# Optimization experiments

Measured on AMD Instinct MI355X. Metric: run time of the kernel, lower is better.

The kernel has to match this reference:

```python
import jax, jax.numpy as jnp
import numpy as np
import math

H = 256
NH = 8
HD = H // NH
FF = 2 * H
NSESS = 8
LN_EPS = 1e-5


def _layernorm(x, g, b):
    m = jnp.mean(x, axis=-1, keepdims=True)
    v = jnp.mean((x - m) ** 2, axis=-1, keepdims=True)
    return (x - m) / jnp.sqrt(v + LN_EPS) * g + b


def setup_inputs() -> dict:
    key = jax.random.key(0)
    ks = jax.random.split(key, 32)
    B, S, N = 4, 256, 32
    inp = {
        'sequence': jax.random.normal(ks[0], (B, S, N, H), dtype=jnp.float32),
        'regime_signal': jax.random.normal(ks[1], (B, S), dtype=jnp.float32),
        'session_transition': jax.random.normal(ks[2], (B, S), dtype=jnp.float32),
    }
    w = lambda k, shape: jax.random.normal(k, shape, dtype=jnp.float32) * 0.02
    inp['q_w'] = w(ks[3], (H, H)); inp['q_b'] = jnp.zeros((H,), jnp.float32)
    inp['k_w'] = w(ks[4], (H, H)); inp['k_b'] = jnp.zeros((H,), jnp.float32)
    inp['v_w'] = w(ks[5], (H, H)); inp['v_b'] = jnp.zeros((H,), jnp.float32)
    inp['o_w'] = w(ks[6], (H, H)); inp['o_b'] = jnp.zeros((H,), jnp.float32)
    inp['sess_emb'] = w(ks[7], (NSESS, H))
    inp['reg_w'] = w(ks[8], (H,)); inp['reg_b'] = jnp.zeros((H,), jnp.float32)
    inp['tr_w'] = w(ks[9], (H,)); inp['tr_b'] = jnp.zeros((H,), jnp.float32)
    inp['tq_w'] = w(ks[10], (H, H)); inp['tq_b'] = jnp.zeros((H,), jnp.float32)
    inp['tk_w'] = w(ks[11], (H, H)); inp['tk_b'] = jnp.zeros((H,), jnp.float32)
    inp['ff_w1'] = w(ks[12], (H, FF)); inp['ff_b1'] = jnp.zeros((FF,), jnp.float32)
    inp['ff_w2'] = w(ks[13], (FF, H)); inp['ff_b2'] = jnp.zeros((H,), jnp.float32)
    inp['ln1_g'] = jnp.ones((H,), jnp.float32); inp['ln1_b'] = jnp.zeros((H,), jnp.float32)
    inp['ln2_g'] = jnp.ones((H,), jnp.float32); inp['ln2_b'] = jnp.zeros((H,), jnp.float32)
    inp['valid_mask'] = jax.random.randint(ks[14], (B, S, N), 0, 2).astype(bool)
    inp['session_codes'] = jax.random.randint(ks[15], (B, S), 0, NSESS).astype(jnp.int64)
    return inp


def _forward(sequence, regime_signal, session_transition,
             q_w, q_b, k_w, k_b, v_w, v_b, o_w, o_b,
             sess_emb, reg_w, reg_b, tr_w, tr_b,
             tq_w, tq_b, tk_w, tk_b,
             ff_w1, ff_b1, ff_w2, ff_b2,
             ln1_g, ln1_b, ln2_g, ln2_b,
             valid_mask, session_codes):
    B, S, N, Hd = sequence.shape
    BN = B * N
    # [B,S,N,H] -> [B*N, S, H]
    flat = sequence.transpose(0, 2, 1, 3).reshape(BN, S, Hd)

    # time-state: session embedding + regime/transition scalar projections
    sess = jnp.clip(session_codes, 0, NSESS - 1)
    sess_flat = jnp.broadcast_to(sess[:, None, :], (B, N, S)).reshape(BN, S)
    time_state = sess_emb[sess_flat]  # [BN, S, H]
    reg_flat = jnp.broadcast_to(regime_signal[:, None, :], (B, N, S)).reshape(BN, S)
    time_state = time_state + reg_flat[..., None] * reg_w + reg_b
    tr_flat = jnp.broadcast_to(session_transition[:, None, :], (B, N, S)).reshape(BN, S)
    time_state = time_state + tr_flat[..., None] * tr_w + tr_b

    def heads(x):  # [BN,S,H] -> [BN,NH,S,HD]
        return x.reshape(BN, S, NH, HD).transpose(0, 2, 1, 3)

    q = heads((flat + time_state) @ q_w + q_b)
    k = heads((flat + time_state) @ k_w + k_b)
    v = heads(flat @ v_w + v_b)
    tq = heads(time_state @ tq_w + tq_b)
    tk = heads(time_state @ tk_w + tk_b)

    scale = 1.0 / math.sqrt(float(HD))
    scores = jnp.einsum('bhqd,bhkd->bhqk', q, k) * scale
    scores = scores + 0.25 * jnp.einsum('bhqd,bhkd->bhqk', tq, tk) * scale

    causal = jnp.triu(jnp.ones((S, S), dtype=bool), k=1)
    scores = jnp.where(causal[None, None], -10000.0, scores)

    valid = valid_mask.transpose(0, 2, 1).reshape(BN, S)  # [BN,S]
    all_invalid = ~jnp.any(valid, axis=1)  # [BN]
    scores = jnp.where(~valid[:, None, None, :], -10000.0, scores)
    first_key = (jnp.arange(S) == 0)
    scores = jnp.where(all_invalid[:, None, None, None] & first_key, 0.0, scores)

    attn = jax.nn.softmax(scores, axis=-1)
    attn = attn * valid[:, None, None, :].astype(attn.dtype)
    attn = attn / jnp.maximum(jnp.sum(attn, axis=-1, keepdims=True), 1e-6)
    attn = jnp.where(all_invalid[:, None, None, None], 0.0, attn)

    attn_out = jnp.einsum('bhqk,bhkd->bhqd', attn, v)
    attn_out = attn_out.transpose(0, 2, 1, 3).reshape(BN, S, Hd)
    attn_out = attn_out @ o_w + o_b

    x = _layernorm(flat + attn_out, ln1_g, ln1_b)  # dropout identity (eval / p=0)
    ff = jax.nn.gelu(x @ ff_w1 + ff_b1, approximate=False) @ ff_w2 + ff_b2
    x = _layernorm(x + ff, ln2_g, ln2_b)
    x = x * valid[..., None].astype(x.dtype)
    return x.reshape(B, N, S, Hd).transpose(0, 2, 1, 3)  # [B,S,N,H]


def reference(sequence, regime_signal, session_transition,
              q_w, q_b, k_w, k_b, v_w, v_b, o_w, o_b,
              sess_emb, reg_w, reg_b, tr_w, tr_b,
              tq_w, tq_b, tk_w, tk_b,
              ff_w1, ff_b1, ff_w2, ff_b2,
              ln1_g, ln1_b, ln2_g, ln2_b,
              valid_mask, session_codes):
    return _forward(sequence, regime_signal, session_transition,
                    q_w, q_b, k_w, k_b, v_w, v_b, o_w, o_b,
                    sess_emb, reg_w, reg_b, tr_w, tr_b,
                    tq_w, tq_b, tk_w, tk_b,
                    ff_w1, ff_b1, ff_w2, ff_b2,
                    ln1_g, ln1_b, ln2_g, ln2_b,
                    valid_mask, session_codes)
```

## Files before the change

### kernel.cpp

```cpp
#include <hip/hip_runtime.h>
#include <math.h>

#define B_ 4
#define S_ 256
#define N_ 32
#define H_ 256
#define NH_ 8
#define HD_ 32
#define FF_ 512
#define BN_ 128
#define M_ 32768
#define BS_ 1024

typedef __attribute__((ext_vector_type(8))) short short8;
typedef __attribute__((ext_vector_type(4))) short short4v;
typedef __attribute__((ext_vector_type(4))) float f32x4;
typedef __attribute__((ext_vector_type(16))) float f32x16;
typedef __attribute__((ext_vector_type(4))) int i32x4;

__device__ __forceinline__ unsigned short f2bf(float f) {
  unsigned u = __builtin_bit_cast(unsigned, f);
  u = (u + 0x7FFFu + ((u >> 16) & 1u)) >> 16;
  return (unsigned short)u;
}
__device__ __forceinline__ float bf2f(unsigned short h) {
  unsigned u = ((unsigned)h) << 16;
  return __builtin_bit_cast(float, u);
}

__device__ __forceinline__ void gload16(const void* g, void* l) {
  __builtin_amdgcn_global_load_lds(
      (const __attribute__((address_space(1))) unsigned*)g,
      (__attribute__((address_space(3))) unsigned*)l, 16, 0, 0);
}

__global__ __launch_bounds__(256)
void cvtts_kernel(const float* __restrict__ q_w, const float* __restrict__ k_w,
                  const float* __restrict__ v_w, const float* __restrict__ o_w,
                  const float* __restrict__ tq_w, const float* __restrict__ tk_w,
                  const float* __restrict__ ff1_w, const float* __restrict__ ff2_w,
                  unsigned short* __restrict__ wqk, unsigned short* __restrict__ wv,
                  unsigned short* __restrict__ wo, unsigned short* __restrict__ wtqtk,
                  unsigned short* __restrict__ wff1, unsigned short* __restrict__ wff2,
                  const float* __restrict__ reg, const float* __restrict__ tr,
                  const int* __restrict__ codes, const float* __restrict__ semb,
                  const float* __restrict__ reg_w, const float* __restrict__ reg_b,
                  const float* __restrict__ tr_w, const float* __restrict__ tr_b,
                  float* __restrict__ ts) {
  const int bid = blockIdx.x, tid = threadIdx.x;
  if (bid >= 2560) {
    const int bs = bid - 2560;
    int c = codes[bs];
    c = c < 0 ? 0 : (c > 7 ? 7 : c);
    const float r = reg[bs], t = tr[bs];
    ts[bs * H_ + tid] = semb[c * H_ + tid] + r * reg_w[tid] + reg_b[tid]
                        + t * tr_w[tid] + tr_b[tid];
    return;
  }
  const float* src; unsigned short* dst; int ns, K, base;
  if (bid < 256)       { src = q_w;   dst = wqk;           ns = 8; K = 256; base = 0; }
  else if (bid < 512)  { src = k_w;   dst = wqk + 65536;   ns = 8; K = 256; base = 256; }
  else if (bid < 768)  { src = v_w;   dst = wv;            ns = 8; K = 256; base = 512; }
  else if (bid < 1024) { src = o_w;   dst = wo;            ns = 8; K = 256; base = 768; }
  else if (bid < 1280) { src = tq_w;  dst = wtqtk;         ns = 8; K = 256; base = 1024; }
  else if (bid < 1536) { src = tk_w;  dst = wtqtk + 65536; ns = 8; K = 256; base = 1280; }
  else if (bid < 2048) { src = ff1_w; dst = wff1;          ns = 9; K = 256; base = 1536; }
  else                 { src = ff2_w; dst = wff2;          ns = 8; K = 512; base = 2048; }
  const int idx = (bid - base) * 256 + tid;
  const int k = idx >> ns, n = idx & ((1 << ns) - 1);
  dst[n * K + k] = f2bf(src[idx]);
}

__global__ __launch_bounds__(256)
void prep_kernel(const float* __restrict__ seq, const float* __restrict__ ts,
                 unsigned short* __restrict__ flatb, unsigned short* __restrict__ fpb) {
  const int row = blockIdx.x * 8 + (threadIdx.x >> 5);
  const int c0 = (threadIdx.x & 31) * 8;
  const int bn = row >> 8, s = row & 255;
  const int b = bn >> 5, n = bn & 31;
  const float* sp = &seq[((((b << 8) + s) << 5) + n) * 256 + c0];
  const float* tp = &ts[(((b << 8) + s) << 8) + c0];
  const float4 a0 = *(const float4*)sp, a1 = *(const float4*)(sp + 4);
  const float4 t0 = *(const float4*)tp, t1 = *(const float4*)(tp + 4);
  short8 fv, gv;
  fv[0] = (short)f2bf(a0.x); fv[1] = (short)f2bf(a0.y);
  fv[2] = (short)f2bf(a0.z); fv[3] = (short)f2bf(a0.w);
  fv[4] = (short)f2bf(a1.x); fv[5] = (short)f2bf(a1.y);
  fv[6] = (short)f2bf(a1.z); fv[7] = (short)f2bf(a1.w);
  gv[0] = (short)f2bf(a0.x + t0.x); gv[1] = (short)f2bf(a0.y + t0.y);
  gv[2] = (short)f2bf(a0.z + t0.z); gv[3] = (short)f2bf(a0.w + t0.w);
  gv[4] = (short)f2bf(a1.x + t1.x); gv[5] = (short)f2bf(a1.y + t1.y);
  gv[6] = (short)f2bf(a1.z + t1.z); gv[7] = (short)f2bf(a1.w + t1.w);
  *(short8*)&flatb[row * 256 + c0] = fv;
  *(short8*)&fpb[row * 256 + c0] = gv;
}

__global__ __launch_bounds__(256)
void proj_kernel(const unsigned short* __restrict__ fpb,
                 const unsigned short* __restrict__ flatb,
                 const float* __restrict__ ts,
                 const unsigned short* __restrict__ wqk,
                 const unsigned short* __restrict__ wv,
                 const unsigned short* __restrict__ wtqtk,
                 const float* __restrict__ q_b, const float* __restrict__ k_b,
                 const float* __restrict__ v_b,
                 const float* __restrict__ tq_b, const float* __restrict__ tk_b,
                 unsigned short* __restrict__ qkb, unsigned short* __restrict__ vb,
                 unsigned short* __restrict__ tqtkb, float c2) {
  __shared__ unsigned short As[128 * 64];
  __shared__ unsigned short Bs[128 * 64];
  const int bid = blockIdx.x, tid = threadIdx.x;
  const int l = tid & 63, w = tid >> 6;
  const int wr = w >> 1, wc = w & 1;
  const int lr = l & 15, lg = l >> 4;

  int region, m0, n0, NOUT;
  const unsigned short* Ab = nullptr;
  const float* Af = nullptr;
  const unsigned short* Wt;
  const float* b0; const float* b1;
  unsigned short* Cv; float scl;
  if (bid < 1024) {
    region = 0; m0 = (bid & 255) * 128; n0 = (bid >> 8) * 128; NOUT = 512;
    Ab = fpb; Wt = wqk; b0 = q_b; b1 = k_b; Cv = qkb; scl = c2;
  } else if (bid < 1536) {
    const int idx = bid - 1024;
    region = 1; m0 = (idx & 255) * 128; n0 = (idx >> 8) * 128; NOUT = 256;
    Ab = flatb; Wt = wv; b0 = v_b; b1 = v_b; Cv = vb; scl = 1.0f;
  } else {
    const int idx = bid - 1536;
    region = 2; m0 = (idx & 7) * 128; n0 = (idx >> 3) * 128; NOUT = 512;
    Af = ts; Wt = wtqtk; b0 = tq_b; b1 = tk_b; Cv = tqtkb; scl = 0.25f * c2;
  }

  f32x4 acc[4][4] = {};
  const unsigned short* ga = (region != 2)
      ? Ab + (m0 + w * 32 + (l >> 3)) * 256 + (l & 7) * 8 : nullptr;
  const unsigned short* gb = Wt + (n0 + w * 32 + (l >> 3)) * 256 + (l & 7) * 8;

  for (int k0 = 0; k0 < 256; k0 += 64) {
    if (region != 2) {
#pragma unroll
      for (int i = 0; i < 4; ++i)
        gload16(ga + k0 + i * 8 * 256, &As[(w * 32 + i * 8) * 64]);
    } else {
#pragma unroll
      for (int i = 0; i < 8; ++i) {
        const int seg = i * 256 + tid;
        const int r = seg >> 4, c4 = (seg & 15) * 4;
        const float4 a4 = *(const float4*)&Af[(m0 + r) * 256 + k0 + c4];
        short4v sv;
        sv[0] = (short)f2bf(a4.x); sv[1] = (short)f2bf(a4.y);
        sv[2] = (short)f2bf(a4.z); sv[3] = (short)f2bf(a4.w);
        *(short4v*)&As[r * 64 + c4] = sv;
      }
    }
#pragma unroll
    for (int i = 0; i < 4; ++i)
      gload16(gb + k0 + i * 8 * 256, &Bs[(w * 32 + i * 8) * 64]);
    __syncthreads();
#pragma unroll
    for (int ks = 0; ks < 2; ++ks) {
      short8 af[4], bfr[4];
#pragma unroll
      for (int qt = 0; qt < 4; ++qt)
        af[qt] = *(const short8*)&As[(wr * 64 + qt * 16 + lr) * 64 + ks * 32 + lg * 8];
#pragma unroll
      for (int nt = 0; nt < 4; ++nt)
        bfr[nt] = *(const short8*)&Bs[(wc * 64 + nt * 16 + lr) * 64 + ks * 32 + lg * 8];
#pragma unroll
      for (int qt = 0; qt < 4; ++qt)
#pragma unroll
        for (int nt = 0; nt < 4; ++nt)
          acc[qt][nt] = __builtin_amdgcn_mfma_f32_16x16x32_bf16(
              af[qt], bfr[nt], acc[qt][nt], 0, 0, 0);
    }
    __syncthreads();
  }

#pragma unroll
  for (int qt = 0; qt < 4; ++qt) {
#pragma unroll
    for (int nt = 0; nt < 4; ++nt) {
      const int col = n0 + wc * 64 + nt * 16 + lr;
      const float bsv = (col < 256) ? b0[col] : b1[col - 256];
      const float sc = (col < 256) ? scl : 1.0f;
#pragma unroll
      for (int i = 0; i < 4; ++i) {
        const int row = m0 + wr * 64 + qt * 16 + (lg << 2) + i;
        Cv[row * NOUT + col] = f2bf((acc[qt][nt][i] + bsv) * sc);
      }
    }
  }
}

template<int K, int NOUT>
__global__ __launch_bounds__(256)
void mmb_kernel(const unsigned short* __restrict__ Ab,
                const unsigned short* __restrict__ Wt,
                const float* __restrict__ bias,
                unsigned short* __restrict__ Cv) {
  __shared__ unsigned short As[128 * 64];
  __shared__ unsigned short Bs[128 * 64];
  const int tid = threadIdx.x;
  const int m0 = blockIdx.x * 128, n0 = blockIdx.y * 128;
  const int l = tid & 63, w = tid >> 6;
  const int wr = w >> 1, wc = w & 1;
  const int lr = l & 15, lg = l >> 4;
  f32x4 acc[4][4] = {};

  const unsigned short* ga = Ab + (m0 + w * 32 + (l >> 3)) * K + (l & 7) * 8;
  const unsigned short* gb = Wt + (n0 + w * 32 + (l >> 3)) * K + (l & 7) * 8;

  for (int k0 = 0; k0 < K; k0 += 64) {
#pragma unroll
    for (int i = 0; i < 4; ++i) {
      gload16(ga + k0 + i * 8 * K, &As[(w * 32 + i * 8) * 64]);
      gload16(gb + k0 + i * 8 * K, &Bs[(w * 32 + i * 8) * 64]);
    }
    __syncthreads();
#pragma unroll
    for (int ks = 0; ks < 2; ++ks) {
      short8 af[4], bfr[4];
#pragma unroll
      for (int qt = 0; qt < 4; ++qt)
        af[qt] = *(const short8*)&As[(wr * 64 + qt * 16 + lr) * 64 + ks * 32 + lg * 8];
#pragma unroll
      for (int nt = 0; nt < 4; ++nt)
        bfr[nt] = *(const short8*)&Bs[(wc * 64 + nt * 16 + lr) * 64 + ks * 32 + lg * 8];
#pragma unroll
      for (int qt = 0; qt < 4; ++qt)
#pragma unroll
        for (int nt = 0; nt < 4; ++nt)
          acc[qt][nt] = __builtin_amdgcn_mfma_f32_16x16x32_bf16(
              af[qt], bfr[nt], acc[qt][nt], 0, 0, 0);
    }
    __syncthreads();
  }

#pragma unroll
  for (int qt = 0; qt < 4; ++qt) {
#pragma unroll
    for (int nt = 0; nt < 4; ++nt) {
      const int col = n0 + wc * 64 + nt * 16 + lr;
      const float bsv = bias[col];
#pragma unroll
      for (int i = 0; i < 4; ++i) {
        const int row = m0 + wr * 64 + qt * 16 + (lg << 2) + i;
        float v = acc[qt][nt][i] + bsv;
        v = 0.5f * v * (1.0f + erff(v * 0.70710678118654752f));
        Cv[row * NOUT + col] = f2bf(v);
      }
    }
  }
}

template<int K, bool FINAL>
__global__ __launch_bounds__(256, 2)
void gemmln_kernel(const unsigned short* __restrict__ Ab,
                   const unsigned short* __restrict__ Wt,
                   const float* __restrict__ bias,
                   const unsigned short* __restrict__ resb,
                   const float* __restrict__ g, const float* __restrict__ bb,
                   const int* __restrict__ valid,
                   void* __restrict__ out) {
  __shared__ unsigned short As[64 * 64];
  __shared__ unsigned short Bs[256 * 64];
  __shared__ float Red[4][64][2];
  const int tid = threadIdx.x;
  const int m0 = blockIdx.x * 64;
  const int l = tid & 63, w = tid >> 6;
  const int lr = l & 15, lg = l >> 4;
  f32x4 acc[4][4] = {};

  const unsigned short* ga = Ab + (m0 + w * 16 + (l >> 3)) * K + (l & 7) * 8;
  const unsigned short* gb = Wt + (w * 64 + (l >> 3)) * K + (l & 7) * 8;

  for (int k0 = 0; k0 < K; k0 += 64) {
#pragma unroll
    for (int i = 0; i < 2; ++i)
      gload16(ga + k0 + i * 8 * K, &As[(w * 16 + i * 8) * 64]);
#pragma unroll
    for (int i = 0; i < 8; ++i)
      gload16(gb + k0 + i * 8 * K, &Bs[(w * 64 + i * 8) * 64]);
    __syncthreads();
#pragma unroll
    for (int ks = 0; ks < 2; ++ks) {
      short8 af[4], bfr[4];
#pragma unroll
      for (int qt = 0; qt < 4; ++qt)
        af[qt] = *(const short8*)&As[(qt * 16 + lr) * 64 + ks * 32 + lg * 8];
#pragma unroll
      for (int nt = 0; nt < 4; ++nt)
        bfr[nt] = *(const short8*)&Bs[(w * 64 + nt * 16 + lr) * 64 + ks * 32 + lg * 8];
#pragma unroll
      for (int qt = 0; qt < 4; ++qt)
#pragma unroll
        for (int nt = 0; nt < 4; ++nt)
          acc[qt][nt] = __builtin_amdgcn_mfma_f32_16x16x32_bf16(
              af[qt], bfr[nt], acc[qt][nt], 0, 0, 0);
    }
    __syncthreads();
  }

#pragma unroll
  for (int qt = 0; qt < 4; ++qt) {
#pragma unroll
    for (int i = 0; i < 4; ++i) {
      const int rl = qt * 16 + (lg << 2) + i;
      const int row = m0 + rl;
      float s1 = 0.0f, s2 = 0.0f;
#pragma unroll
      for (int nt = 0; nt < 4; ++nt) {
        const int col = w * 64 + nt * 16 + lr;
        float v = acc[qt][nt][i] + bias[col] + bf2f(resb[row * 256 + col]);
        acc[qt][nt][i] = v;
        s1 += v; s2 += v * v;
      }
      s1 += __shfl_xor(s1, 1); s2 += __shfl_xor(s2, 1);
      s1 += __shfl_xor(s1, 2); s2 += __shfl_xor(s2, 2);
      s1 += __shfl_xor(s1, 4); s2 += __shfl_xor(s2, 4);
      s1 += __shfl_xor(s1, 8); s2 += __shfl_xor(s2, 8);
      if (lr == 0) { Red[w][rl][0] = s1; Red[w][rl][1] = s2; }
    }
  }
  __syncthreads();

#pragma unroll
  for (int qt = 0; qt < 4; ++qt) {
#pragma unroll
    for (int i = 0; i < 4; ++i) {
      const int rl = qt * 16 + (lg << 2) + i;
      const int row = m0 + rl;
      const float s1 = (Red[0][rl][0] + Red[1][rl][0])
                     + (Red[2][rl][0] + Red[3][rl][0]);
      const float s2 = (Red[0][rl][1] + Red[1][rl][1])
                     + (Red[2][rl][1] + Red[3][rl][1]);
      const float mean = s1 * (1.0f / 256.0f);
      const float var = s2 * (1.0f / 256.0f) - mean * mean;
      const float rstd = rsqrtf(var + 1e-5f);
      if (FINAL) {
        const int bn = row >> 8, s = row & 255;
        const int b = bn >> 5, n = bn & 31;
        const float vm = (valid[((b << 8) + s) * 32 + n] != 0) ? 1.0f : 0.0f;
        float* op = (float*)out + ((((b << 8) + s) << 5) + n) * 256;
#pragma unroll
        for (int nt = 0; nt < 4; ++nt) {
          const int col = w * 64 + nt * 16 + lr;
          op[col] = ((acc[qt][nt][i] - mean) * rstd * g[col] + bb[col]) * vm;
        }
      } else {
        unsigned short* op = (unsigned short*)out + row * 256;
#pragma unroll
        for (int nt = 0; nt < 4; ++nt) {
          const int col = w * 64 + nt * 16 + lr;
          op[col] = f2bf((acc[qt][nt][i] - mean) * rstd * g[col] + bb[col]);
        }
      }
    }
  }
}

__device__ __forceinline__ void attn_group(
    const int kbase, const int qa, const int hi, const int lq,
    const short8* __restrict__ qf,
    const char* __restrict__ KsB, const char* __restrict__ VsB,
    const unsigned long long bm0, const unsigned long long bm1,
    const unsigned long long bm2, const unsigned long long bm3,
    f32x16& oacc, float& lrun) {
  f32x16 s = {};
#pragma unroll
  for (int df = 0; df < 4; ++df) {
    const int key = kbase + lq;
    const short8 akf = *(const short8*)(
        KsB + key * 128 + ((df * 32 + hi * 16) ^ ((key & 7) << 4)));
    s = __builtin_amdgcn_mfma_f32_32x32x16_bf16(akf, qf[df], s, 0, 0, 0);
  }
  const unsigned long long bmc = (kbase < 64) ? bm0 : (kbase < 128) ? bm1
                               : (kbase < 192) ? bm2 : bm3;
  const unsigned wnd = (kbase & 32) ? (unsigned)(bmc >> 32) : (unsigned)bmc;
  float p[16];
#pragma unroll
  for (int r = 0; r < 16; ++r) {
    const int crow = (r & 3) + 8 * (r >> 2) + 4 * hi;
    const int key = kbase + crow;
    const bool ok = (key <= qa) && (((wnd >> crow) & 1u) != 0u);
    p[r] = ok ? __builtin_amdgcn_exp2f(s[r]) : 0.0f;
  }
  float rs = ((p[0] + p[1]) + (p[2] + p[3])) + ((p[4] + p[5]) + (p[6] + p[7]))
           + ((p[8] + p[9]) + (p[10] + p[11])) + ((p[12] + p[13]) + (p[14] + p[15]));
  rs += __shfl_xor(rs, 32);
  lrun += rs;
  unsigned wds[8];
#pragma unroll
  for (int i2 = 0; i2 < 8; ++i2)
    wds[i2] = (unsigned)f2bf(p[2 * i2]) | ((unsigned)f2bf(p[2 * i2 + 1]) << 16);
  unsigned xw[8];
#pragma unroll
  for (int i2 = 0; i2 < 8; ++i2)
    xw[i2] = (unsigned)__shfl_xor((int)wds[i2], 32);
  i32x4 f0, f1;
  f0[0] = (int)(hi ? xw[2] : wds[0]);
  f0[1] = (int)(hi ? xw[3] : wds[1]);
  f0[2] = (int)(hi ? wds[2] : xw[0]);
  f0[3] = (int)(hi ? wds[3] : xw[1]);
  f1[0] = (int)(hi ? xw[6] : wds[4]);
  f1[1] = (int)(hi ? xw[7] : wds[5]);
  f1[2] = (int)(hi ? wds[6] : xw[4]);
  f1[3] = (int)(hi ? wds[7] : xw[5]);
  const short8 pf0 = __builtin_bit_cast(short8, f0);
  const short8 pf1 = __builtin_bit_cast(short8, f1);
  {
    const short8 avf = *(const short8*)(
        VsB + lq * 512 + (((kbase + hi * 8) * 2) ^ ((lq & 7) << 4)));
    oacc = __builtin_amdgcn_mfma_f32_32x32x16_bf16(avf, pf0, oacc, 0, 0, 0);
  }
  {
    const short8 avf = *(const short8*)(
        VsB + lq * 512 + (((kbase + 16 + hi * 8) * 2) ^ ((lq & 7) << 4)));
    oacc = __builtin_amdgcn_mfma_f32_32x32x16_bf16(avf, pf1, oacc, 0, 0, 0);
  }
}

__global__ __launch_bounds__(512, 4)
void attn6_kernel(const unsigned short* __restrict__ qkb,
                  const unsigned short* __restrict__ vb,
                  const unsigned short* __restrict__ tqtkb,
                  const int* __restrict__ valid,
                  unsigned short* __restrict__ ao) {
  __shared__ __align__(16) char KsB[256 * 128];
  __shared__ __align__(16) char VsB[32 * 512];

  const int bn = blockIdx.x & 127;
  const int h = blockIdx.x >> 7;
  const int b = bn >> 5, n = bn & 31;
  const int tid = threadIdx.x, l = tid & 63, w = tid >> 6;
  const int lq = l & 31, hi = l >> 5;
  const int qa = w * 32 + lq;

  const unsigned long long bm0 = __ballot(valid[((b << 8) + 0   + l) * 32 + n] != 0);
  const unsigned long long bm1 = __ballot(valid[((b << 8) + 64  + l) * 32 + n] != 0);
  const unsigned long long bm2 = __ballot(valid[((b << 8) + 128 + l) * 32 + n] != 0);
  const unsigned long long bm3 = __ballot(valid[((b << 8) + 192 + l) * 32 + n] != 0);

  short8 qf[4];
  {
    const unsigned short* qp = &qkb[((bn << 8) + qa) * 512 + (h << 5)];
    const unsigned short* tp = &tqtkb[((b << 8) + qa) * 512 + (h << 5)];
    qf[0] = *(const short8*)&qp[hi * 8];
    qf[1] = *(const short8*)&qp[16 + hi * 8];
    qf[2] = *(const short8*)&tp[hi * 8];
    qf[3] = *(const short8*)&tp[16 + hi * 8];
  }

  {
    const int cp = (l & 7) ^ (l >> 3);
    const unsigned short* base0 = (cp < 4)
        ? &qkb[((bn << 8) + (l >> 3)) * 512 + 256 + (h << 5) + cp * 8]
        : &tqtkb[((b << 8) + (l >> 3)) * 512 + 256 + (h << 5) + (cp - 4) * 8];
#pragma unroll
    for (int i = 0; i < 4; ++i) {
      const int kb0 = i * 64 + w * 8;
      gload16(base0 + kb0 * 512, KsB + kb0 * 128);
    }
  }
#pragma unroll
  for (int i = 0; i < 2; ++i) {
    const int e = i * 512 + tid;
    const int key = e >> 2, c = e & 3;
    const short8 v = *(const short8*)&vb[((bn << 8) + key) * 256 + (h << 5) + c * 8];
#pragma unroll
    for (int j = 0; j < 8; ++j) {
      const int dv = c * 8 + j;
      *(unsigned short*)(VsB + dv * 512 + ((key * 2) ^ ((dv & 7) << 4))) =
          (unsigned short)v[j];
    }
  }
  __syncthreads();

  f32x16 oacc = {}, oacc2 = {};
  float lrun = 0.0f, lrun2 = 0.0f;

  const int gstart = (w >= 4) ? (w - 3) : 0;
  for (int g = gstart; g <= w; ++g)
    attn_group(g << 5, qa, hi, lq, qf, KsB, VsB, bm0, bm1, bm2, bm3, oacc, lrun);

  if (w < 4) {
    const int ch = 7 - w;
    const int qa2 = ch * 32 + lq;
    short8 qf2[4];
    const unsigned short* qp = &qkb[((bn << 8) + qa2) * 512 + (h << 5)];
    const unsigned short* tp = &tqtkb[((b << 8) + qa2) * 512 + (h << 5)];
    qf2[0] = *(const short8*)&qp[hi * 8];
    qf2[1] = *(const short8*)&qp[16 + hi * 8];
    qf2[2] = *(const short8*)&tp[hi * 8];
    qf2[3] = *(const short8*)&tp[16 + hi * 8];
    for (int g = 0; g <= ch - 4; ++g)
      attn_group(g << 5, qa2, hi, lq, qf2, KsB, VsB, bm0, bm1, bm2, bm3,
                 oacc2, lrun2);
  }

  __syncthreads();
  if (w < 4) {
    float* mo = (float*)(KsB + w * 4096);
#pragma unroll
    for (int r = 0; r < 16; ++r) mo[r * 64 + l] = oacc2[r];
    ((float*)(KsB + 16384))[w * 64 + l] = lrun2;
  }
  __syncthreads();
  if (w >= 4) {
    const float* mo = (const float*)(KsB + (7 - w) * 4096);
#pragma unroll
    for (int r = 0; r < 16; ++r) oacc[r] += mo[r * 64 + l];
    lrun += ((const float*)(KsB + 16384))[(7 - w) * 64 + l];
  }

  const float inv = 1.0f / fmaxf(lrun, 1e-6f);
  const int row = (bn << 8) + qa;
#pragma unroll
  for (int g2 = 0; g2 < 4; ++g2) {
    const unsigned long long h0 = f2bf(oacc[4 * g2 + 0] * inv);
    const unsigned long long h1 = f2bf(oacc[4 * g2 + 1] * inv);
    const unsigned long long h2 = f2bf(oacc[4 * g2 + 2] * inv);
    const unsigned long long h3 = f2bf(oacc[4 * g2 + 3] * inv);
    const unsigned long long pkt = h0 | (h1 << 16) | (h2 << 32) | (h3 << 48);
    *(unsigned long long*)&ao[row * 256 + (h << 5) + 8 * g2 + 4 * hi] = pkt;
  }
}

extern "C" void kernel_launch(void* const* d_in, const int* in_sizes, int n_in,
                              void* d_out, int out_size, void* d_ws, size_t ws_size,
                              hipStream_t stream) {
  const float* seq    = (const float*)d_in[0];
  const float* regs   = (const float*)d_in[1];
  const float* trs    = (const float*)d_in[2];
  const float* q_w    = (const float*)d_in[3];
  const float* q_b    = (const float*)d_in[4];
  const float* k_w    = (const float*)d_in[5];
  const float* k_b    = (const float*)d_in[6];
  const float* v_w    = (const float*)d_in[7];
  const float* v_b    = (const float*)d_in[8];
  const float* o_w    = (const float*)d_in[9];
  const float* o_b    = (const float*)d_in[10];
  const float* semb   = (const float*)d_in[11];
  const float* reg_w  = (const float*)d_in[12];
  const float* reg_b  = (const float*)d_in[13];
  const float* tr_w   = (const float*)d_in[14];
  const float* tr_b   = (const float*)d_in[15];
  const float* tq_w   = (const float*)d_in[16];
  const float* tq_b   = (const float*)d_in[17];
  const float* tk_w   = (const float*)d_in[18];
  const float* tk_b   = (const float*)d_in[19];
  const float* ff_w1  = (const float*)d_in[20];
  const float* ff_b1  = (const float*)d_in[21];
  const float* ff_w2  = (const float*)d_in[22];
  const float* ff_b2  = (const float*)d_in[23];
  const float* ln1_g  = (const float*)d_in[24];
  const float* ln1_b  = (const float*)d_in[25];
  const float* ln2_g  = (const float*)d_in[26];
  const float* ln2_b  = (const float*)d_in[27];
  const int*   valid  = (const int*)d_in[28];
  const int*   codes  = (const int*)d_in[29];

  float* f32ws = (float*)d_ws;
  float* ts    = f32ws;
  unsigned short* bws = (unsigned short*)(f32ws + 262144 + 8388608);
  unsigned short* flatb = bws;
  unsigned short* fpb   = bws + 8388608;
  unsigned short* qkb   = bws + 16777216;
  unsigned short* vb    = bws + 33554432;
  unsigned short* tqtkb = bws + 41943040;
  unsigned short* wqk   = bws + 42467328;
  unsigned short* wv    = bws + 42598400;
  unsigned short* wo    = bws + 42663936;
  unsigned short* wtqtk = bws + 42729472;
  unsigned short* wff1  = bws + 42860544;
  unsigned short* wff2  = bws + 42991616;
  unsigned short* ao  = fpb;
  unsigned short* x1b = flatb;
  unsigned short* h1  = qkb;
  float* outp = (float*)d_out;

  const float c2 = 0.25505402f;

  cvtts_kernel<<<3584, 256, 0, stream>>>(
      q_w, k_w, v_w, o_w, tq_w, tk_w, ff_w1, ff_w2,
      wqk, wv, wo, wtqtk, wff1, wff2,
      regs, trs, codes, semb, reg_w, reg_b, tr_w, tr_b, ts);
  prep_kernel<<<M_ / 8, 256, 0, stream>>>(seq, ts, flatb, fpb);
  proj_kernel<<<1568, 256, 0, stream>>>(
      fpb, flatb, ts, wqk, wv, wtqtk,
      q_b, k_b, v_b, tq_b, tk_b, qkb, vb, tqtkb, c2);
  attn6_kernel<<<BN_ * NH_, 512, 0, stream>>>(qkb, vb, tqtkb, valid, ao);
  gemmln_kernel<256, false><<<M_ / 64, 256, 0, stream>>>(
      ao, wo, o_b, flatb, ln1_g, ln1_b, nullptr, x1b);
  mmb_kernel<256, 512><<<dim3(256, 4), 256, 0, stream>>>(x1b, wff1, ff_b1, h1);
  gemmln_kernel<512, true><<<M_ / 64, 256, 0, stream>>>(
      h1, wff2, ff_b2, x1b, ln2_g, ln2_b, valid, outp);
}
```

Baseline: 163.9 us.

## Fuse prep into weight-conversion kernel and XOR-swizzle GEMM shared-memory tiles

After: 158.7 us (median of 2 runs). 1.03x faster.

```diff
diff --git a/kernel.cpp b/kernel.cpp
--- a/kernel.cpp
+++ b/kernel.cpp
@@ -46,8 +46,36 @@
                   const int* __restrict__ codes, const float* __restrict__ semb,
                   const float* __restrict__ reg_w, const float* __restrict__ reg_b,
                   const float* __restrict__ tr_w, const float* __restrict__ tr_b,
-                  float* __restrict__ ts) {
+                  float* __restrict__ ts,
+                  const float* __restrict__ seq,
+                  unsigned short* __restrict__ flatb,
+                  unsigned short* __restrict__ fpb) {
   const int bid = blockIdx.x, tid = threadIdx.x;
+  if (bid >= 3584) {
+    const int row = (bid - 3584) * 8 + (tid >> 5);
+    const int c0 = (tid & 31) * 8;
+    const int bn = row >> 8, s = row & 255;
+    const int b = bn >> 5, n = bn & 31;
+    const int bs = (b << 8) + s;
+    int c = codes[bs];
+    c = c < 0 ? 0 : (c > 7 ? 7 : c);
+    const float r = reg[bs], t = tr[bs];
+    const float* sp = &seq[(((bs << 5)) + n) * 256 + c0];
+    const float4 a0 = *(const float4*)sp, a1 = *(const float4*)(sp + 4);
+    short8 fv, gv;
+    float av[8] = {a0.x, a0.y, a0.z, a0.w, a1.x, a1.y, a1.z, a1.w};
+#pragma unroll
+    for (int j = 0; j < 8; ++j) {
+      const int hcol = c0 + j;
+      const float tsv = semb[c * H_ + hcol] + r * reg_w[hcol] + reg_b[hcol]
+                        + t * tr_w[hcol] + tr_b[hcol];
+      fv[j] = (short)f2bf(av[j]);
+      gv[j] = (short)f2bf(av[j] + tsv);
+    }
+    *(short8*)&flatb[row * 256 + c0] = fv;
+    *(short8*)&fpb[row * 256 + c0] = gv;
+    return;
+  }
   if (bid >= 2560) {
     const int bs = bid - 2560;
     int c = codes[bs];
@@ -69,30 +97,6 @@
   const int idx = (bid - base) * 256 + tid;
   const int k = idx >> ns, n = idx & ((1 << ns) - 1);
   dst[n * K + k] = f2bf(src[idx]);
-}
-
-__global__ __launch_bounds__(256)
-void prep_kernel(const float* __restrict__ seq, const float* __restrict__ ts,
-                 unsigned short* __restrict__ flatb, unsigned short* __restrict__ fpb) {
-  const int row = blockIdx.x * 8 + (threadIdx.x >> 5);
-  const int c0 = (threadIdx.x & 31) * 8;
-  const int bn = row >> 8, s = row & 255;
-  const int b = bn >> 5, n = bn & 31;
-  const float* sp = &seq[((((b << 8) + s) << 5) + n) * 256 + c0];
-  const float* tp = &ts[(((b << 8) + s) << 8) + c0];
-  const float4 a0 = *(const float4*)sp, a1 = *(const float4*)(sp + 4);
-  const float4 t0 = *(const float4*)tp, t1 = *(const float4*)(tp + 4);
-  short8 fv, gv;
-  fv[0] = (short)f2bf(a0.x); fv[1] = (short)f2bf(a0.y);
-  fv[2] = (short)f2bf(a0.z); fv[3] = (short)f2bf(a0.w);
-  fv[4] = (short)f2bf(a1.x); fv[5] = (short)f2bf(a1.y);
-  fv[6] = (short)f2bf(a1.z); fv[7] = (short)f2bf(a1.w);
-  gv[0] = (short)f2bf(a0.x + t0.x); gv[1] = (short)f2bf(a0.y + t0.y);
-  gv[2] = (short)f2bf(a0.z + t0.z); gv[3] = (short)f2bf(a0.w + t0.w);
-  gv[4] = (short)f2bf(a1.x + t1.x); gv[5] = (short)f2bf(a1.y + t1.y);
-  gv[6] = (short)f2bf(a1.z + t1.z); gv[7] = (short)f2bf(a1.w + t1.w);
-  *(short8*)&flatb[row * 256 + c0] = fv;
-  *(short8*)&fpb[row * 256 + c0] = gv;
 }
 
 __global__ __launch_bounds__(256)
@@ -113,6 +117,7 @@
   const int l = tid & 63, w = tid >> 6;
   const int wr = w >> 1, wc = w & 1;
   const int lr = l & 15, lg = l >> 4;
+  const int sw = (lr & 7) << 3;
 
   int region, m0, n0, NOUT;
   const unsigned short* Ab = nullptr;
@@ -134,9 +139,10 @@
   }
 
   f32x4 acc[4][4] = {};
+  const int cg = (l & 7) ^ (l >> 3);
   const unsigned short* ga = (region != 2)
-      ? Ab + (m0 + w * 32 + (l >> 3)) * 256 + (l & 7) * 8 : nullptr;
-  const unsigned short* gb = Wt + (n0 + w * 32 + (l >> 3)) * 256 + (l & 7) * 8;
+      ? Ab + (m0 + w * 32 + (l >> 3)) * 256 + cg * 8 : nullptr;
+  const unsigned short* gb = Wt + (n0 + w * 32 + (l >> 3)) * 256 + cg * 8;
 
   for (int k0 = 0; k0 < 256; k0 += 64) {
     if (region != 2) {
@@ -152,7 +158,7 @@
         short4v sv;
         sv[0] = (short)f2bf(a4.x); sv[1] = (short)f2bf(a4.y);
         sv[2] = (short)f2bf(a4.z); sv[3] = (short)f2bf(a4.w);
-        *(short4v*)&As[r * 64 + c4] = sv;
+        *(short4v*)&As[r * 64 + (c4 ^ ((r & 7) << 3))] = sv;
       }
     }
 #pragma unroll
@@ -164,10 +170,12 @@
       short8 af[4], bfr[4];
 #pragma unroll
       for (int qt = 0; qt < 4; ++qt)
-        af[qt] = *(const short8*)&As[(wr * 64 + qt * 16 + lr) * 64 + ks * 32 + lg * 8];
+        af[qt] = *(const short8*)&As[(wr * 64 + qt * 16 + lr) * 64
+                                     + ((ks * 32 + lg * 8) ^ sw)];
 #pragma unroll
       for (int nt = 0; nt < 4; ++nt)
-        bfr[nt] = *(const short8*)&Bs[(wc * 64 + nt * 16 + lr) * 64 + ks * 32 + lg * 8];
+        bfr[nt] = *(const short8*)&Bs[(wc * 64 + nt * 16 + lr) * 64
+                                      + ((ks * 32 + lg * 8) ^ sw)];
 #pragma unroll
       for (int qt = 0; qt < 4; ++qt)
 #pragma unroll
@@ -207,10 +215,12 @@
   const int l = tid & 63, w = tid >> 6;
   const int wr = w >> 1, wc = w & 1;
   const int lr = l & 15, lg = l >> 4;
+  const int sw = (lr & 7) << 3;
   f32x4 acc[4][4] = {};
 
-  const unsigned short* ga = Ab + (m0 + w * 32 + (l >> 3)) * K + (l & 7) * 8;
-  const unsigned short* gb = Wt + (n0 + w * 32 + (l >> 3)) * K + (l & 7) * 8;
+  const int cg = (l & 7) ^ (l >> 3);
+  const unsigned short* ga = Ab + (m0 + w * 32 + (l >> 3)) * K + cg * 8;
+  const unsigned short* gb = Wt + (n0 + w * 32 + (l >> 3)) * K + cg * 8;
 
   for (int k0 = 0; k0 < K; k0 += 64) {
 #pragma unroll
@@ -224,10 +234,12 @@
       short8 af[4], bfr[4];
 #pragma unroll
       for (int qt = 0; qt < 4; ++qt)
-        af[qt] = *(const short8*)&As[(wr * 64 + qt * 16 + lr) * 64 + ks * 32 + lg * 8];
+        af[qt] = *(const short8*)&As[(wr * 64 + qt * 16 + lr) * 64
+                                     + ((ks * 32 + lg * 8) ^ sw)];
 #pragma unroll
       for (int nt = 0; nt < 4; ++nt)
-        bfr[nt] = *(const short8*)&Bs[(wc * 64 + nt * 16 + lr) * 64 + ks * 32 + lg * 8];
+        bfr[nt] = *(const short8*)&Bs[(wc * 64 + nt * 16 + lr) * 64
+                                      + ((ks * 32 + lg * 8) ^ sw)];
 #pragma unroll
       for (int qt = 0; qt < 4; ++qt)
 #pragma unroll
@@ -583,11 +595,11 @@
 
   const float c2 = 0.25505402f;
 
-  cvtts_kernel<<<3584, 256, 0, stream>>>(
+  cvtts_kernel<<<7680, 256, 0, stream>>>(
       q_w, k_w, v_w, o_w, tq_w, tk_w, ff_w1, ff_w2,
       wqk, wv, wo, wtqtk, wff1, wff2,
-      regs, trs, codes, semb, reg_w, reg_b, tr_w, tr_b, ts);
-  prep_kernel<<<M_ / 8, 256, 0, stream>>>(seq, ts, flatb, fpb);
+      regs, trs, codes, semb, reg_w, reg_b, tr_w, tr_b, ts,
+      seq, flatb, fpb);
   proj_kernel<<<1568, 256, 0, stream>>>(
       fpb, flatb, ts, wqk, wv, wtqtk,
       q_b, k_b, v_b, tq_b, tk_b, qkb, vb, tqtkb, c2);
```
